# Kernel tuning notes

Hardware: AMD Instinct MI355X
Metric: run time of the kernel (lower is better)

## Reference

```python
import jax, jax.numpy as jnp
import numpy as np

B, M, Wc, K, IN = 32, 65536, 64, 8, 512
R = K + 1                      # sparse_reads + last_used slot
IFACE = 2 * Wc + R + 1         # interface_size = 2w + r + 1


def setup_inputs() -> dict:
    key = jax.random.key(0)
    ks = jax.random.split(key, 8)
    xi = jax.random.normal(ks[0], (B, IN), jnp.float32)
    sparse = jax.random.normal(ks[1], (B, M, Wc), jnp.float32)
    read_weights = jax.random.uniform(ks[2], (B, 1, R), jnp.float32)
    read_vectors = jax.random.normal(ks[3], (B, R, Wc), jnp.float32)
    W = jax.random.normal(ks[4], (IN, IFACE), jnp.float32) / np.sqrt(IN).astype(np.float32)
    b = jnp.zeros((IFACE,), jnp.float32)
    read_positions = jax.random.randint(ks[5], (B, R), 0, M, dtype=jnp.int32)
    last_used_mem = jax.random.randint(ks[6], (B,), 0, M, dtype=jnp.int32)
    return dict(xi=xi, sparse=sparse, read_weights=read_weights,
                read_vectors=read_vectors, W=W, b=b,
                read_positions=read_positions, last_used_mem=last_used_mem)


def reference(xi, sparse, read_weights, read_vectors, W, b, read_positions, last_used_mem):
    bsz = xi.shape[0]
    w, r, m, k = Wc, R, M, K
    # interface linear (independent_linears=False path)
    iface = xi @ W + b                                   # [b, 2w+r+1]
    read_query = iface[:, :w]                            # [b, w]
    write_vector = iface[:, w:2 * w][:, None, :]         # [b, 1, w]
    ig = iface[:, 2 * w:2 * w + r][:, None, :]           # [b, 1, r]
    write_gate = jax.nn.sigmoid(iface[:, -1])[:, None, None]  # [b, 1, 1]
    # write(): interpolate read weights, rank-1 update of read_vectors
    ww = write_gate * (ig * read_weights + (1.0 - ig))   # [b, 1, r]
    rv = read_vectors + jnp.einsum('bor,bow->brw', ww, write_vector)  # [b, r, w]
    # write_into_memory(): for l in range(b): sparse[:, positions[l], :] = rv
    flat_pos = read_positions.reshape(-1)                # [b*r]
    flat_k = jnp.tile(jnp.arange(r, dtype=jnp.int32), bsz)
    order = jnp.full((m,), -1, jnp.int32).at[flat_pos].max(
        jnp.arange(bsz * r, dtype=jnp.int32))            # last writer per slot
    k_final = flat_k[order[flat_pos]]                    # winning k per written entry
    sparse = sparse.at[:, flat_pos, :].set(rv[:, k_final, :])
    # read_from_sparse_memory(): brute-force exact KNN (squared L2, replaces FLANN kd-tree)
    d = (jnp.sum(sparse * sparse, -1)
         - 2.0 * jnp.einsum('bmw,bw->bm', sparse, read_query)
         + jnp.sum(read_query * read_query, -1, keepdims=True))  # [b, m]
    neg_d, pos = jax.lax.top_k(-d, k)                    # k nearest
    dist = -neg_d                                        # [b, k]
    pos = jnp.concatenate([pos.astype(jnp.int32), last_used_mem[:, None]], axis=1)  # [b, r]
    dist = jnp.concatenate([dist, jnp.zeros((bsz, 1), dist.dtype)], axis=1)          # [b, r]
    dist = dist / jnp.max(dist, axis=1, keepdims=True)   # distances / max(distances)
    gathered = jnp.take_along_axis(sparse, pos[:, :, None], axis=1)  # [b, r, w]
    read_weights_new = dist[:, None, :]                  # [b, 1, r]
    return gathered[:, :k, :], read_weights_new, gathered
```

## Files before the change

### kernel.cpp

```cpp
#include <hip/hip_runtime.h>
#include <float.h>
#include <math.h>

#define Bz    32
#define Mz    65536
#define WCz   64
#define Rz    9
#define INz   512
#define IFz   138
#define NBLK  64
#define RPB   1024


__device__ __forceinline__ bool pless(float d1, int i1, float d2, int i2) {
    return (d1 < d2) || (d1 == d2 && i1 < i2);
}

__global__ __launch_bounds__(256) void k_prep(
    const float* __restrict__ xi, const float* __restrict__ W,
    const float* __restrict__ bias,
    const float* __restrict__ read_weights,
    const float* __restrict__ read_vectors,
    const int*   __restrict__ read_positions,
    float* __restrict__ ws_q, float* __restrict__ ws_qq,
    float* __restrict__ ws_rv, float* __restrict__ ws_dv,
    int* __restrict__ ws_wpos, int* __restrict__ ws_wk, int* __restrict__ ws_nw)
{
    __shared__ float xs[INz];
    __shared__ float if_s[IFz];
    __shared__ float ww_s[Rz];
    __shared__ float rv_s[Rz * WCz];
    __shared__ float qq_s;
    __shared__ int   pos_s[Bz * Rz];
    __shared__ int   nw_s;

    int t = threadIdx.x, b = blockIdx.x;
    for (int i = t; i < INz / 4; i += 256)
        ((float4*)xs)[i] = ((const float4*)(xi + (size_t)b * INz))[i];
    for (int i = t; i < Bz * Rz; i += 256) pos_s[i] = read_positions[i];
    if (t == 0) nw_s = 0;
    __syncthreads();

    if (t < IFz) {
        float a0 = 0.f, a1 = 0.f, a2 = 0.f, a3 = 0.f;
        #pragma unroll 4
        for (int i = 0; i < INz; i += 4) {
            a0 = fmaf(xs[i + 0], W[(i + 0) * IFz + t], a0);
            a1 = fmaf(xs[i + 1], W[(i + 1) * IFz + t], a1);
            a2 = fmaf(xs[i + 2], W[(i + 2) * IFz + t], a2);
            a3 = fmaf(xs[i + 3], W[(i + 3) * IFz + t], a3);
        }
        if_s[t] = (a0 + a1) + (a2 + a3) + bias[t];
    }
    __syncthreads();

    if (t < 64) {
        float v = if_s[t];
        ws_q[b * WCz + t] = v;
        float p = v * v;
        p += __shfl_xor(p, 1);  p += __shfl_xor(p, 2);  p += __shfl_xor(p, 4);
        p += __shfl_xor(p, 8);  p += __shfl_xor(p, 16); p += __shfl_xor(p, 32);
        if (t == 0) { qq_s = p; ws_qq[b] = p; }
    } else if (t < 64 + Rz) {
        int r = t - 64;
        float g  = 1.0f / (1.0f + expf(-if_s[IFz - 1]));
        float ig = if_s[2 * WCz + r];
        ww_s[r] = g * (ig * read_weights[b * Rz + r] + (1.0f - ig));
    }
    __syncthreads();

    for (int i = t; i < Rz * WCz; i += 256) {
        int r = i >> 6, w = i & 63;
        float v = fmaf(ww_s[r], if_s[WCz + w], read_vectors[(size_t)b * Rz * WCz + i]);
        rv_s[i] = v;
        ws_rv[(size_t)b * Rz * WCz + i] = v;
    }

    if (b == 0) {
        for (int i = t; i < Bz * Rz; i += 256) {
            int p = pos_s[i];
            bool win = true;
            for (int j = i + 1; j < Bz * Rz; j++)
                if (pos_s[j] == p) { win = false; break; }
            if (win) {
                int slot = atomicAdd(&nw_s, 1);
                ws_wpos[slot] = p;
                ws_wk[slot]   = i % Rz;
            }
        }
    }
    __syncthreads();

    if (t < Rz) {
        float s1 = 0.f, s2 = 0.f;
        for (int w = 0; w < WCz; w++) {
            float v = rv_s[t * WCz + w];
            s1 = fmaf(v, v, s1);
            s2 = fmaf(v, if_s[w], s2);
        }
        ws_dv[b * Rz + t] = s1 - 2.0f * s2 + qq_s;
    }
    if (b == 0 && t == 0) ws_nw[0] = nw_s;
}

__global__ __launch_bounds__(256) void k_dist(
    const float* __restrict__ sparse,
    const float* __restrict__ ws_q, const float* __restrict__ ws_qq,
    const int* __restrict__ read_positions,
    float* __restrict__ cand_d, int* __restrict__ cand_i)
{
    __shared__ float d_s[RPB];
    __shared__ unsigned int bmp[RPB / 32];
    __shared__ float md[64 * 8];
    __shared__ int   mi[64 * 8];

    int t = threadIdx.x;
    int b = blockIdx.y;
    int chunk = blockIdx.x;
    int lo = chunk * RPB;

    if (t < RPB / 32) bmp[t] = 0u;
    __syncthreads();
    for (int i = t; i < Bz * Rz; i += 256) {
        int rel = read_positions[i] - lo;
        if ((unsigned)rel < (unsigned)RPB) atomicOr(&bmp[rel >> 5], 1u << (rel & 31));
    }

    int e = t & 15;
    int g = t >> 4;
    const float4 q4 = *(const float4*)(ws_q + b * WCz + e * 4);
    float m0 = -2.f * q4.x, m1 = -2.f * q4.y, m2 = -2.f * q4.z, m3 = -2.f * q4.w;
    float qq = ws_qq[b];
    const float* base = sparse + ((size_t)b * Mz + lo) * WCz + e * 4;
    __syncthreads();

    #pragma unroll 1
    for (int it = 0; it < RPB / 16; it += 8) {
        float4 f[8];
        int rl[8];
        #pragma unroll
        for (int u = 0; u < 8; u++) {
            rl[u] = (it + u) * 16 + g;
            f[u] = *(const float4*)(base + (size_t)rl[u] * WCz);
        }
        #pragma unroll
        for (int u = 0; u < 8; u++) {
            float p = f[u].x * (f[u].x + m0);
            p = fmaf(f[u].y, f[u].y + m1, p);
            p = fmaf(f[u].z, f[u].z + m2, p);
            p = fmaf(f[u].w, f[u].w + m3, p);
            p += __shfl_xor(p, 1);
            p += __shfl_xor(p, 2);
            p += __shfl_xor(p, 4);
            p += __shfl_xor(p, 8);
            if (e == 0) {
                float d = p + qq;
                int r = rl[u];
                if ((bmp[r >> 5] >> (r & 31)) & 1u) d = FLT_MAX;
                d_s[r] = d;
            }
        }
    }
    __syncthreads();

    if (t < 64) {
        float ld[8]; int li[8];
        #pragma unroll
        for (int k = 0; k < 8; k++) { ld[k] = FLT_MAX; li[k] = 0x7FFFFFFF; }
        for (int r = t; r < RPB; r += 64) {
            float v = d_s[r];
            int idx = lo + r;
            if (pless(v, idx, ld[7], li[7])) {
                #pragma unroll
                for (int k = 7; k >= 0; k--) {
                    bool ltp = (k > 0) && pless(v, idx, ld[k - 1], li[k - 1]);
                    bool lth = pless(v, idx, ld[k], li[k]);
                    if (lth) {
                        if (ltp) { ld[k] = ld[k - 1]; li[k] = li[k - 1]; }
                        else     { ld[k] = v;         li[k] = idx; }
                    }
                }
            }
        }
        #pragma unroll
        for (int k = 0; k < 8; k++) { md[t * 8 + k] = ld[k]; mi[t * 8 + k] = li[k]; }
    }
    __syncthreads();
    for (int step = 32; step >= 1; step >>= 1) {
        if (t < step) {
            float od[8]; int oi[8];
            int ia = 0, ib = 0;
            #pragma unroll
            for (int k = 0; k < 8; k++) {
                float da = md[t * 8 + ia],        db = md[(t + step) * 8 + ib];
                int   ja = mi[t * 8 + ia],        jb = mi[(t + step) * 8 + ib];
                if (pless(da, ja, db, jb)) { od[k] = da; oi[k] = ja; ia++; }
                else                       { od[k] = db; oi[k] = jb; ib++; }
            }
            #pragma unroll
            for (int k = 0; k < 8; k++) { md[t * 8 + k] = od[k]; mi[t * 8 + k] = oi[k]; }
        }
        __syncthreads();
    }
    if (t < 8) {
        cand_d[((size_t)b * NBLK + chunk) * 8 + t] = md[t];
        cand_i[((size_t)b * NBLK + chunk) * 8 + t] = mi[t];
    }
}

__global__ __launch_bounds__(256) void k_final(
    const float* __restrict__ sparse,
    const int* __restrict__ last_used,
    const float* __restrict__ ws_rv, const float* __restrict__ ws_dv,
    const int* __restrict__ ws_wpos, const int* __restrict__ ws_wk,
    const int* __restrict__ ws_nw,
    const float* __restrict__ cand_d, const int* __restrict__ cand_i,
    float* __restrict__ out)
{
    __shared__ float cd[1024]; __shared__ int ci[1024];
    __shared__ float md[64 * 8]; __shared__ int mi[64 * 8];
    __shared__ int pos_s[Rz]; __shared__ float dist_s[Rz]; __shared__ int fk_s[Rz];

    int t = threadIdx.x;
    int b = blockIdx.x;
    int nw = ws_nw[0];

    for (int i = t; i < NBLK * 8; i += 256) {
        cd[i] = cand_d[(size_t)b * NBLK * 8 + i];
        ci[i] = cand_i[(size_t)b * NBLK * 8 + i];
    }
    for (int i = t; i < nw; i += 256) {
        cd[NBLK * 8 + i] = ws_dv[b * Rz + ws_wk[i]];
        ci[NBLK * 8 + i] = ws_wpos[i];
    }
    for (int i = NBLK * 8 + nw + t; i < 1024; i += 256) { cd[i] = FLT_MAX; ci[i] = 0x7FFFFFFF; }
    __syncthreads();

    if (t < 64) {
        float ld[8]; int li[8];
        #pragma unroll
        for (int k = 0; k < 8; k++) { ld[k] = FLT_MAX; li[k] = 0x7FFFFFFF; }
        for (int r = t; r < 1024; r += 64) {
            float v = cd[r]; int idx = ci[r];
            if (pless(v, idx, ld[7], li[7])) {
                #pragma unroll
                for (int k = 7; k >= 0; k--) {
                    bool ltp = (k > 0) && pless(v, idx, ld[k - 1], li[k - 1]);
                    bool lth = pless(v, idx, ld[k], li[k]);
                    if (lth) {
                        if (ltp) { ld[k] = ld[k - 1]; li[k] = li[k - 1]; }
                        else     { ld[k] = v;         li[k] = idx; }
                    }
                }
            }
        }
        #pragma unroll
        for (int k = 0; k < 8; k++) { md[t * 8 + k] = ld[k]; mi[t * 8 + k] = li[k]; }
    }
    __syncthreads();
    for (int step = 32; step >= 1; step >>= 1) {
        if (t < step) {
            float od[8]; int oi[8];
            int ia = 0, ib = 0;
            #pragma unroll
            for (int k = 0; k < 8; k++) {
                float da = md[t * 8 + ia],        db = md[(t + step) * 8 + ib];
                int   ja = mi[t * 8 + ia],        jb = mi[(t + step) * 8 + ib];
                if (pless(da, ja, db, jb)) { od[k] = da; oi[k] = ja; ia++; }
                else                       { od[k] = db; oi[k] = jb; ib++; }
            }
            #pragma unroll
            for (int k = 0; k < 8; k++) { md[t * 8 + k] = od[k]; mi[t * 8 + k] = oi[k]; }
        }
        __syncthreads();
    }

    if (t == 0) {
        float norm = 0.f;
        for (int j = 0; j < 8; j++) { dist_s[j] = md[j]; pos_s[j] = mi[j]; norm = fmaxf(norm, md[j]); }
        dist_s[8] = 0.f;
        pos_s[8]  = last_used[b];
        for (int j = 0; j < Rz; j++)
            out[Bz * 8 * WCz + b * Rz + j] = dist_s[j] / norm;
    }
    __syncthreads();

    if (t < Rz) {
        int p = pos_s[t]; int fk = -1;
        for (int i = 0; i < nw; i++)
            if (ws_wpos[i] == p) { fk = ws_wk[i]; break; }
        fk_s[t] = fk;
    }
    __syncthreads();

    for (int i = t; i < Rz * WCz; i += 256) {
        int j = i >> 6, w = i & 63;
        int p = pos_s[j]; int fk = fk_s[j];
        float v = (fk >= 0) ? ws_rv[(b * Rz + fk) * WCz + w]
                            : sparse[((size_t)b * Mz + p) * WCz + w];
        out[Bz * 8 * WCz + Bz * Rz + (b * Rz + j) * WCz + w] = v;
        if (j < 8) out[(b * 8 + j) * WCz + w] = v;
    }
}

extern "C" void kernel_launch(void* const* d_in, const int* in_sizes, int n_in,
                              void* d_out, int out_size, void* d_ws, size_t ws_size,
                              hipStream_t stream) {
    const float* xi             = (const float*)d_in[0];
    const float* sparse         = (const float*)d_in[1];
    const float* read_weights   = (const float*)d_in[2];
    const float* read_vectors   = (const float*)d_in[3];
    const float* W              = (const float*)d_in[4];
    const float* bias           = (const float*)d_in[5];
    const int*   read_positions = (const int*)d_in[6];
    const int*   last_used      = (const int*)d_in[7];
    float* out = (float*)d_out;
    float* ws  = (float*)d_ws;

    float* ws_q    = ws + 4416;
    float* ws_qq   = ws + 6464;
    float* ws_rv   = ws + 6496;
    float* ws_dv   = ws + 24928;
    int*   ws_wpos = (int*)(ws + 25216);
    int*   ws_wk   = (int*)(ws + 25504);
    int*   ws_nw   = (int*)(ws + 25792);
    float* cand_d  = ws + 25796;
    int*   cand_i  = (int*)(ws + 42180);

    k_prep<<<dim3(Bz), dim3(256), 0, stream>>>(xi, W, bias, read_weights,
                                               read_vectors, read_positions,
                                               ws_q, ws_qq, ws_rv, ws_dv,
                                               ws_wpos, ws_wk, ws_nw);
    k_dist<<<dim3(NBLK, Bz), dim3(256), 0, stream>>>(sparse, ws_q, ws_qq,
                                                     read_positions, cand_d, cand_i);
    k_final<<<dim3(Bz), dim3(256), 0, stream>>>(sparse, last_used, ws_rv, ws_dv,
                                                ws_wpos, ws_wk, ws_nw, cand_d,
                                                cand_i, out);
}
```

Measured before the change: 783.6 us.

## Shrink prep kernel to query only, move write logic to final, pipeline distance loads

The prep kernel now computes only the read query and its squared norm, splitting the 512-long dot product across four thread groups. The rest of the interface columns, the read-vector update, the dedup of write positions and the write distances move into the final kernel, all kept in shared memory. The distance kernel now gives each row to 4 lanes instead of 16, with each lane loading four float4s, and double-buffers register loads so the next rows are in flight while the current ones are reduced. The goal is a shorter critical path before the memory-bound scan and more loads in flight, at the cost of more registers and extra work in the final kernel.

```diff
diff --git a/kernel.cpp b/kernel.cpp
--- a/kernel.cpp
+++ b/kernel.cpp
@@ -11,96 +11,44 @@
 #define NBLK  64
 #define RPB   1024
 
+typedef float f32x4 __attribute__((ext_vector_type(4)));
+
 
 __device__ __forceinline__ bool pless(float d1, int i1, float d2, int i2) {
     return (d1 < d2) || (d1 == d2 && i1 < i2);
 }
 
-__global__ __launch_bounds__(256) void k_prep(
+__global__ __launch_bounds__(256) void k_q(
     const float* __restrict__ xi, const float* __restrict__ W,
     const float* __restrict__ bias,
-    const float* __restrict__ read_weights,
-    const float* __restrict__ read_vectors,
-    const int*   __restrict__ read_positions,
-    float* __restrict__ ws_q, float* __restrict__ ws_qq,
-    float* __restrict__ ws_rv, float* __restrict__ ws_dv,
-    int* __restrict__ ws_wpos, int* __restrict__ ws_wk, int* __restrict__ ws_nw)
+    float* __restrict__ ws_q, float* __restrict__ ws_qq)
 {
     __shared__ float xs[INz];
-    __shared__ float if_s[IFz];
-    __shared__ float ww_s[Rz];
-    __shared__ float rv_s[Rz * WCz];
-    __shared__ float qq_s;
-    __shared__ int   pos_s[Bz * Rz];
-    __shared__ int   nw_s;
-
+    __shared__ float red[256];
     int t = threadIdx.x, b = blockIdx.x;
     for (int i = t; i < INz / 4; i += 256)
         ((float4*)xs)[i] = ((const float4*)(xi + (size_t)b * INz))[i];
-    for (int i = t; i < Bz * Rz; i += 256) pos_s[i] = read_positions[i];
-    if (t == 0) nw_s = 0;
-    __syncthreads();
-
-    if (t < IFz) {
-        float a0 = 0.f, a1 = 0.f, a2 = 0.f, a3 = 0.f;
-        #pragma unroll 4
-        for (int i = 0; i < INz; i += 4) {
-            a0 = fmaf(xs[i + 0], W[(i + 0) * IFz + t], a0);
-            a1 = fmaf(xs[i + 1], W[(i + 1) * IFz + t], a1);
-            a2 = fmaf(xs[i + 2], W[(i + 2) * IFz + t], a2);
-            a3 = fmaf(xs[i + 3], W[(i + 3) * IFz + t], a3);
-        }
-        if_s[t] = (a0 + a1) + (a2 + a3) + bias[t];
-    }
-    __syncthreads();
-
+    __syncthreads();
+
+    int j = t & 63, s = t >> 6;
+    float a0 = 0.f, a1 = 0.f, a2 = 0.f, a3 = 0.f;
+    #pragma unroll 4
+    for (int i = s * 128; i < s * 128 + 128; i += 4) {
+        a0 = fmaf(xs[i + 0], W[(i + 0) * IFz + j], a0);
+        a1 = fmaf(xs[i + 1], W[(i + 1) * IFz + j], a1);
+        a2 = fmaf(xs[i + 2], W[(i + 2) * IFz + j], a2);
+        a3 = fmaf(xs[i + 3], W[(i + 3) * IFz + j], a3);
+    }
+    red[t] = (a0 + a1) + (a2 + a3);
+    __syncthreads();
     if (t < 64) {
-        float v = if_s[t];
+        float v = ((red[t] + red[t + 64]) + (red[t + 128] + red[t + 192])) + bias[t];
         ws_q[b * WCz + t] = v;
         float p = v * v;
         p += __shfl_xor(p, 1);  p += __shfl_xor(p, 2);  p += __shfl_xor(p, 4);
         p += __shfl_xor(p, 8);  p += __shfl_xor(p, 16); p += __shfl_xor(p, 32);
-        if (t == 0) { qq_s = p; ws_qq[b] = p; }
-    } else if (t < 64 + Rz) {
-        int r = t - 64;
-        float g  = 1.0f / (1.0f + expf(-if_s[IFz - 1]));
-        float ig = if_s[2 * WCz + r];
-        ww_s[r] = g * (ig * read_weights[b * Rz + r] + (1.0f - ig));
-    }
-    __syncthreads();
-
-    for (int i = t; i < Rz * WCz; i += 256) {
-        int r = i >> 6, w = i & 63;
-        float v = fmaf(ww_s[r], if_s[WCz + w], read_vectors[(size_t)b * Rz * WCz + i]);
-        rv_s[i] = v;
-        ws_rv[(size_t)b * Rz * WCz + i] = v;
-    }
-
-    if (b == 0) {
-        for (int i = t; i < Bz * Rz; i += 256) {
-            int p = pos_s[i];
-            bool win = true;
-            for (int j = i + 1; j < Bz * Rz; j++)
-                if (pos_s[j] == p) { win = false; break; }
-            if (win) {
-                int slot = atomicAdd(&nw_s, 1);
-                ws_wpos[slot] = p;
-                ws_wk[slot]   = i % Rz;
-            }
-        }
-    }
-    __syncthreads();
-
-    if (t < Rz) {
-        float s1 = 0.f, s2 = 0.f;
-        for (int w = 0; w < WCz; w++) {
-            float v = rv_s[t * WCz + w];
-            s1 = fmaf(v, v, s1);
-            s2 = fmaf(v, if_s[w], s2);
-        }
-        ws_dv[b * Rz + t] = s1 - 2.0f * s2 + qq_s;
-    }
-    if (b == 0 && t == 0) ws_nw[0] = nw_s;
+        if (t == 0) ws_qq[b] = p;
+    }
 }
 
 __global__ __launch_bounds__(256) void k_dist(
@@ -126,36 +74,93 @@
         if ((unsigned)rel < (unsigned)RPB) atomicOr(&bmp[rel >> 5], 1u << (rel & 31));
     }
 
-    int e = t & 15;
-    int g = t >> 4;
-    const float4 q4 = *(const float4*)(ws_q + b * WCz + e * 4);
-    float m0 = -2.f * q4.x, m1 = -2.f * q4.y, m2 = -2.f * q4.z, m3 = -2.f * q4.w;
+    int e = t & 3;
+    int g = t >> 2;
+    f32x4 m[4];
+    #pragma unroll
+    for (int j = 0; j < 4; j++) {
+        f32x4 qv = *(const f32x4*)(ws_q + b * WCz + j * 16 + e * 4);
+        m[j] = -2.f * qv;
+    }
     float qq = ws_qq[b];
-    const float* base = sparse + ((size_t)b * Mz + lo) * WCz + e * 4;
-    __syncthreads();
+    const f32x4* base4 = (const f32x4*)(sparse + ((size_t)b * Mz + lo) * WCz);
+    __syncthreads();
+
+    f32x4 A[8], Bv[8];
+    #pragma unroll
+    for (int u = 0; u < 2; u++)
+        #pragma unroll
+        for (int j = 0; j < 4; j++)
+            A[u * 4 + j] = base4[(size_t)(u * 64 + g) * 16 + j * 4 + e];
 
     #pragma unroll 1
-    for (int it = 0; it < RPB / 16; it += 8) {
-        float4 f[8];
-        int rl[8];
-        #pragma unroll
-        for (int u = 0; u < 8; u++) {
-            rl[u] = (it + u) * 16 + g;
-            f[u] = *(const float4*)(base + (size_t)rl[u] * WCz);
-        }
-        #pragma unroll
-        for (int u = 0; u < 8; u++) {
-            float p = f[u].x * (f[u].x + m0);
-            p = fmaf(f[u].y, f[u].y + m1, p);
-            p = fmaf(f[u].z, f[u].z + m2, p);
-            p = fmaf(f[u].w, f[u].w + m3, p);
-            p += __shfl_xor(p, 1);
-            p += __shfl_xor(p, 2);
-            p += __shfl_xor(p, 4);
-            p += __shfl_xor(p, 8);
+    for (int s = 0; s < 16; s += 4) {
+        #pragma unroll
+        for (int u = 0; u < 2; u++)
+            #pragma unroll
+            for (int j = 0; j < 4; j++)
+                Bv[u * 4 + j] = base4[(size_t)((s + 2 + u) * 64 + g) * 16 + j * 4 + e];
+        #pragma unroll
+        for (int u = 0; u < 2; u++) {
+            const f32x4* F = &A[u * 4];
+            float p0 = F[0].x * (F[0].x + m[0].x);
+            p0 = fmaf(F[0].y, F[0].y + m[0].y, p0);
+            p0 = fmaf(F[0].z, F[0].z + m[0].z, p0);
+            p0 = fmaf(F[0].w, F[0].w + m[0].w, p0);
+            float p1 = F[1].x * (F[1].x + m[1].x);
+            p1 = fmaf(F[1].y, F[1].y + m[1].y, p1);
+            p1 = fmaf(F[1].z, F[1].z + m[1].z, p1);
+            p1 = fmaf(F[1].w, F[1].w + m[1].w, p1);
+            float p2 = F[2].x * (F[2].x + m[2].x);
+            p2 = fmaf(F[2].y, F[2].y + m[2].y, p2);
+            p2 = fmaf(F[2].z, F[2].z + m[2].z, p2);
+            p2 = fmaf(F[2].w, F[2].w + m[2].w, p2);
+            float p3 = F[3].x * (F[3].x + m[3].x);
+            p3 = fmaf(F[3].y, F[3].y + m[3].y, p3);
+            p3 = fmaf(F[3].z, F[3].z + m[3].z, p3);
+            p3 = fmaf(F[3].w, F[3].w + m[3].w, p3);
+            float acc = (p0 + p1) + (p2 + p3);
+            acc += __shfl_xor(acc, 1);
+            acc += __shfl_xor(acc, 2);
             if (e == 0) {
-                float d = p + qq;
-                int r = rl[u];
+                int r = (s + u) * 64 + g;
+                float d = acc + qq;
+                if ((bmp[r >> 5] >> (r & 31)) & 1u) d = FLT_MAX;
+                d_s[r] = d;
+            }
+        }
+        if (s + 4 < 16) {
+            #pragma unroll
+            for (int u = 0; u < 2; u++)
+                #pragma unroll
+                for (int j = 0; j < 4; j++)
+                    A[u * 4 + j] = base4[(size_t)((s + 4 + u) * 64 + g) * 16 + j * 4 + e];
+        }
+        #pragma unroll
+        for (int u = 0; u < 2; u++) {
+            const f32x4* F = &Bv[u * 4];
+            float p0 = F[0].x * (F[0].x + m[0].x);
+            p0 = fmaf(F[0].y, F[0].y + m[0].y, p0);
+            p0 = fmaf(F[0].z, F[0].z + m[0].z, p0);
+            p0 = fmaf(F[0].w, F[0].w + m[0].w, p0);
+            float p1 = F[1].x * (F[1].x + m[1].x);
+            p1 = fmaf(F[1].y, F[1].y + m[1].y, p1);
+            p1 = fmaf(F[1].z, F[1].z + m[1].z, p1);
+            p1 = fmaf(F[1].w, F[1].w + m[1].w, p1);
+            float p2 = F[2].x * (F[2].x + m[2].x);
+            p2 = fmaf(F[2].y, F[2].y + m[2].y, p2);
+            p2 = fmaf(F[2].z, F[2].z + m[2].z, p2);
+            p2 = fmaf(F[2].w, F[2].w + m[2].w, p2);
+            float p3 = F[3].x * (F[3].x + m[3].x);
+            p3 = fmaf(F[3].y, F[3].y + m[3].y, p3);
+            p3 = fmaf(F[3].z, F[3].z + m[3].z, p3);
+            p3 = fmaf(F[3].w, F[3].w + m[3].w, p3);
+            float acc = (p0 + p1) + (p2 + p3);
+            acc += __shfl_xor(acc, 1);
+            acc += __shfl_xor(acc, 2);
+            if (e == 0) {
+                int r = (s + 2 + u) * 64 + g;
+                float d = acc + qq;
                 if ((bmp[r >> 5] >> (r & 31)) & 1u) d = FLT_MAX;
                 d_s[r] = d;
             }
@@ -210,28 +215,101 @@
 
 __global__ __launch_bounds__(256) void k_final(
     const float* __restrict__ sparse,
+    const float* __restrict__ xi, const float* __restrict__ W,
+    const float* __restrict__ bias,
+    const float* __restrict__ read_weights,
+    const float* __restrict__ read_vectors,
+    const int* __restrict__ read_positions,
     const int* __restrict__ last_used,
-    const float* __restrict__ ws_rv, const float* __restrict__ ws_dv,
-    const int* __restrict__ ws_wpos, const int* __restrict__ ws_wk,
-    const int* __restrict__ ws_nw,
+    const float* __restrict__ ws_q, const float* __restrict__ ws_qq,
     const float* __restrict__ cand_d, const int* __restrict__ cand_i,
     float* __restrict__ out)
 {
+    __shared__ float xs[INz];
+    __shared__ float red[256];
+    __shared__ float if2_s[80];
+    __shared__ float ww_s[Rz];
+    __shared__ float rv_s[Rz * WCz];
+    __shared__ float dv_s[Rz];
+    __shared__ int   pos_all[Bz * Rz];
+    __shared__ int   wpos_s[Bz * Rz];
+    __shared__ int   wk_s[Bz * Rz];
+    __shared__ int   nw_s;
     __shared__ float cd[1024]; __shared__ int ci[1024];
     __shared__ float md[64 * 8]; __shared__ int mi[64 * 8];
     __shared__ int pos_s[Rz]; __shared__ float dist_s[Rz]; __shared__ int fk_s[Rz];
 
     int t = threadIdx.x;
     int b = blockIdx.x;
-    int nw = ws_nw[0];
-
+
+    for (int i = t; i < INz / 4; i += 256)
+        ((float4*)xs)[i] = ((const float4*)(xi + (size_t)b * INz))[i];
+    for (int i = t; i < Bz * Rz; i += 256) pos_all[i] = read_positions[i];
+    if (t == 0) nw_s = 0;
+    __syncthreads();
+
+    {
+        int col = 64 + (t & 127);
+        int half = t >> 7;
+        float a0 = 0.f, a1 = 0.f, a2 = 0.f, a3 = 0.f;
+        if ((t & 127) < 74) {
+            #pragma unroll 4
+            for (int i = half * 256; i < half * 256 + 256; i += 4) {
+                a0 = fmaf(xs[i + 0], W[(i + 0) * IFz + col], a0);
+                a1 = fmaf(xs[i + 1], W[(i + 1) * IFz + col], a1);
+                a2 = fmaf(xs[i + 2], W[(i + 2) * IFz + col], a2);
+                a3 = fmaf(xs[i + 3], W[(i + 3) * IFz + col], a3);
+            }
+        }
+        red[t] = (a0 + a1) + (a2 + a3);
+    }
+    __syncthreads();
+    if (t < 74) if2_s[t] = red[t] + red[t + 128] + bias[64 + t];
+    __syncthreads();
+
+    if (t < Rz) {
+        float g  = 1.0f / (1.0f + expf(-if2_s[73]));
+        float ig = if2_s[64 + t];
+        ww_s[t] = g * (ig * read_weights[b * Rz + t] + (1.0f - ig));
+    }
+    __syncthreads();
+
+    for (int i = t; i < Rz * WCz; i += 256) {
+        int r = i >> 6, w = i & 63;
+        rv_s[i] = fmaf(ww_s[r], if2_s[w], read_vectors[(size_t)b * Rz * WCz + i]);
+    }
+    for (int i = t; i < Bz * Rz; i += 256) {
+        int p = pos_all[i];
+        bool win = true;
+        for (int j = i + 1; j < Bz * Rz; j++)
+            if (pos_all[j] == p) { win = false; break; }
+        if (win) {
+            int slot = atomicAdd(&nw_s, 1);
+            wpos_s[slot] = p;
+            wk_s[slot]   = i % Rz;
+        }
+    }
     for (int i = t; i < NBLK * 8; i += 256) {
         cd[i] = cand_d[(size_t)b * NBLK * 8 + i];
         ci[i] = cand_i[(size_t)b * NBLK * 8 + i];
     }
+    __syncthreads();
+
+    if (t < Rz) {
+        float s1 = 0.f, s2 = 0.f;
+        for (int w = 0; w < WCz; w++) {
+            float v = rv_s[t * WCz + w];
+            s1 = fmaf(v, v, s1);
+            s2 = fmaf(v, ws_q[b * WCz + w], s2);
+        }
+        dv_s[t] = s1 - 2.0f * s2 + ws_qq[b];
+    }
+    __syncthreads();
+
+    int nw = nw_s;
     for (int i = t; i < nw; i += 256) {
-        cd[NBLK * 8 + i] = ws_dv[b * Rz + ws_wk[i]];
-        ci[NBLK * 8 + i] = ws_wpos[i];
+        cd[NBLK * 8 + i] = dv_s[wk_s[i]];
+        ci[NBLK * 8 + i] = wpos_s[i];
     }
     for (int i = NBLK * 8 + nw + t; i < 1024; i += 256) { cd[i] = FLT_MAX; ci[i] = 0x7FFFFFFF; }
     __syncthreads();
@@ -288,7 +366,7 @@
     if (t < Rz) {
         int p = pos_s[t]; int fk = -1;
         for (int i = 0; i < nw; i++)
-            if (ws_wpos[i] == p) { fk = ws_wk[i]; break; }
+            if (wpos_s[i] == p) { fk = wk_s[i]; break; }
         fk_s[t] = fk;
     }
     __syncthreads();
@@ -296,7 +374,7 @@
     for (int i = t; i < Rz * WCz; i += 256) {
         int j = i >> 6, w = i & 63;
         int p = pos_s[j]; int fk = fk_s[j];
-        float v = (fk >= 0) ? ws_rv[(b * Rz + fk) * WCz + w]
+        float v = (fk >= 0) ? rv_s[fk * WCz + w]
                             : sparse[((size_t)b * Mz + p) * WCz + w];
         out[Bz * 8 * WCz + Bz * Rz + (b * Rz + j) * WCz + w] = v;
         if (j < 8) out[(b * 8 + j) * WCz + w] = v;
@@ -317,23 +395,16 @@
     float* out = (float*)d_out;
     float* ws  = (float*)d_ws;
 
-    float* ws_q    = ws + 4416;
-    float* ws_qq   = ws + 6464;
-    float* ws_rv   = ws + 6496;
-    float* ws_dv   = ws + 24928;
-    int*   ws_wpos = (int*)(ws + 25216);
-    int*   ws_wk   = (int*)(ws + 25504);
-    int*   ws_nw   = (int*)(ws + 25792);
-    float* cand_d  = ws + 25796;
-    int*   cand_i  = (int*)(ws + 42180);
-
-    k_prep<<<dim3(Bz), dim3(256), 0, stream>>>(xi, W, bias, read_weights,
-                                               read_vectors, read_positions,
-                                               ws_q, ws_qq, ws_rv, ws_dv,
-                                               ws_wpos, ws_wk, ws_nw);
+    float* ws_q    = ws + 0;
+    float* ws_qq   = ws + 2048;
+    float* cand_d  = ws + 2080;
+    int*   cand_i  = (int*)(ws + 18464);
+
+    k_q<<<dim3(Bz), dim3(256), 0, stream>>>(xi, W, bias, ws_q, ws_qq);
     k_dist<<<dim3(NBLK, Bz), dim3(256), 0, stream>>>(sparse, ws_q, ws_qq,
                                                      read_positions, cand_d, cand_i);
-    k_final<<<dim3(Bz), dim3(256), 0, stream>>>(sparse, last_used, ws_rv, ws_dv,
-                                                ws_wpos, ws_wk, ws_nw, cand_d,
-                                                cand_i, out);
+    k_final<<<dim3(Bz), dim3(256), 0, stream>>>(sparse, xi, W, bias, read_weights,
+                                                read_vectors, read_positions,
+                                                last_used, ws_q, ws_qq,
+                                                cand_d, cand_i, out);
 }
```

Measured after the change: 777.8 us. About the same (-0.7%).
